# Optimization experiments

Measured on AMD Instinct MI355X. Metric: run time of the kernel, lower is better.

Reference implementation:

```python
import jax, jax.numpy as jnp
import numpy as np

N, R, IN_DIM, OUT_DIM, MODE = 8, 256, 64, 64, 32


def setup_inputs() -> dict:
    key = jax.random.key(0)
    k_x, k_w0, k_w1, k_rw, k_rb = jax.random.split(key, 5)
    scale = (1.0 / (IN_DIM * OUT_DIM)) * np.sqrt(IN_DIM + OUT_DIM)
    return {
        "x": jax.random.normal(k_x, (N, R, R, IN_DIM), dtype=jnp.float32),
        # real/imag stacked, matching torch Parameter [m, m, in, out, 2]
        "w0": jax.random.normal(k_w0, (MODE, MODE, IN_DIM, OUT_DIM, 2), dtype=jnp.float32) * scale,
        "w1": jax.random.normal(k_w1, (MODE, MODE, IN_DIM, OUT_DIM, 2), dtype=jnp.float32) * scale,
        # residual Linear: stored as [in, out] (torch keeps [out, in]; math identical)
        "res_w": jax.random.normal(k_rw, (IN_DIM, OUT_DIM), dtype=jnp.float32) * 0.05,
        "res_b": jax.random.normal(k_rb, (OUT_DIM,), dtype=jnp.float32) * 0.05,
    }


def reference(x, w0, w1, res_w, res_b):
    n, r, _, in_dim = x.shape
    m = w0.shape[0]
    rc = r // 2 + 1
    out_dim = w0.shape[3]

    # residual branch (Linear)
    res = jnp.einsum("nhwi,io->nhwo", x, res_w) + res_b  # [N, r, r, out]

    # channels-first for 2D FFT over spatial dims (droprate = 0 -> no dropout)
    xt = jnp.transpose(x, (0, 3, 1, 2))                    # [N, in, r, r]
    x_ft = jnp.fft.rfft2(xt, s=(r, r), norm="ortho")       # [N, in, r, rc] complex

    # gather low-frequency mode blocks: rows [0:m] and [r-m:r], cols [0:m]
    blk0 = x_ft[:, :, :m, :m]                              # [N, in, m, m]
    blk1 = x_ft[:, :, r - m:, :m]                          # [N, in, m, m]

    W0 = w0[..., 0] + 1j * w0[..., 1]                      # [m, m, in, out]
    W1 = w1[..., 0] + 1j * w1[..., 1]

    out0 = jnp.einsum("nixy,xyio->noxy", blk0, W0)         # [N, out, m, m]
    out1 = jnp.einsum("nixy,xyio->noxy", blk1, W1)

    # scatter back into zero-initialized full spectrum
    out_ft = jnp.zeros((n, out_dim, r, rc), dtype=out0.dtype)
    out_ft = out_ft.at[:, :, :m, :m].set(out0)
    out_ft = out_ft.at[:, :, r - m:, :m].set(out1)

    y = jnp.fft.irfft2(out_ft, s=(r, r), norm="ortho")     # [N, out, r, r]
    y = jnp.transpose(y, (0, 2, 3, 1))                     # [N, r, r, out]
    return jax.nn.silu(y + res)
```

## Files before the change

### kernel.cpp

```cpp
#include <hip/hip_runtime.h>
#include <math.h>

#define NN 8
#define RR 256
#define CD 64
#define MM 32
#define KHN 64
#define KWN 32

#define ANG 0.024543692606170259f
#define INVN (1.0f / 65536.0f)

typedef __attribute__((ext_vector_type(4))) float f32x4;
typedef __attribute__((ext_vector_type(8))) short short8;
typedef unsigned short u16;

__device__ inline u16 f2bf(float f) {
    union { float f; unsigned u; } v; v.f = f;
    unsigned r = v.u + 0x7FFF + ((v.u >> 16) & 1);
    return (u16)(r >> 16);
}
__device__ inline unsigned pack2(float a, float b) {
    return (unsigned)f2bf(a) | ((unsigned)f2bf(b) << 16);
}

__global__ __launch_bounds__(256) void k0_tables(u16* __restrict__ A2g,
                                                 u16* __restrict__ A4g,
                                                 u16* __restrict__ T1g,
                                                 u16* __restrict__ T5g) {
    int gid = blockIdx.x * 256 + threadIdx.x;
    {
        int r = gid >> 9, k = gid & 511;
        int khIdx = r & 63, part = r >> 6;
        int kh = (khIdx < 32) ? khIdx : 192 + khIdx;
        int h = k & 255, kpart = k >> 8;
        float s, c;
        __sincosf((float)((kh * h) & 255) * ANG, &s, &c);
        float v = (part == 0) ? ((kpart == 0) ? c : s)
                              : ((kpart == 0) ? -s : c);
        A2g[gid] = f2bf(v);
    }
    {
        int r = gid >> 7, k = gid & 127;
        int h = r & 255, part = r >> 8;
        int khIdx = k & 63, kpart = k >> 6;
        int kh = (khIdx < 32) ? khIdx : 192 + khIdx;
        float s, c;
        __sincosf((float)((kh * h) & 255) * ANG, &s, &c);
        float v = (part == 0) ? ((kpart == 0) ? c : -s)
                              : ((kpart == 0) ? s : c);
        A4g[gid] = f2bf(v);
    }
    if (gid < 16384) {
        {
            int r = gid >> 8, w = gid & 255;
            float s, c;
            if (r < 32) { __sincosf((float)((r * w) & 255) * ANG, &s, &c); T1g[gid] = f2bf(c); }
            else        { __sincosf((float)(((r - 32) * w) & 255) * ANG, &s, &c); T1g[gid] = f2bf(-s); }
        }
        {
            int w = gid >> 6, c = gid & 63;
            float v;
            if (c == 0) v = 1.0f;
            else if (c < 32) { float s, co; __sincosf((float)((c * w) & 255) * ANG, &s, &co); v = 2.0f * co; }
            else if (c == 32) v = 0.0f;
            else { float s, co; __sincosf((float)(((c - 32) * w) & 255) * ANG, &s, &co); v = -2.0f * s; }
            T5g[gid] = f2bf(v);
        }
    }
}

__global__ __launch_bounds__(256) void k1_dft_w(const float* __restrict__ x,
                                                const u16* __restrict__ T1g,
                                                u16* __restrict__ X1R,
                                                u16* __restrict__ X1I) {
    __shared__ __align__(16) u16 At[64 * 264];
    __shared__ __align__(16) u16 Bt[64 * 264];
    int t = threadIdx.x;
    int nh = blockIdx.x;
#pragma unroll
    for (int it = 0; it < 8; ++it) {
        int idx = t + it * 256;
        int row = idx >> 5, oct = idx & 31;
        *(uint4*)&At[row * 264 + oct * 8] = *(const uint4*)&T1g[row * 256 + oct * 8];
    }
    const float* xr = x + (size_t)nh * (RR * CD);
#pragma unroll
    for (int it = 0; it < 32; ++it) {
        int idx = t + it * 256;
        int q = idx >> 6, cc = idx & 63;
        float f0 = xr[(2 * q) * 64 + cc];
        float f1 = xr[(2 * q + 1) * 64 + cc];
        ((unsigned*)Bt)[(cc * 264 + 2 * q) >> 1] = pack2(f0, f1);
    }
    __syncthreads();
    int wv = t >> 6, l = t & 63, lm = l & 15, lq = l >> 4;
    f32x4 acc[4];
#pragma unroll
    for (int nt = 0; nt < 4; ++nt) { f32x4 z = {0.f, 0.f, 0.f, 0.f}; acc[nt] = z; }
#pragma unroll
    for (int ks = 0; ks < 8; ++ks) {
        short8 a = *(const short8*)&At[(wv * 16 + lm) * 264 + ks * 32 + lq * 8];
#pragma unroll
        for (int nt = 0; nt < 4; ++nt) {
            short8 b = *(const short8*)&Bt[(nt * 16 + lm) * 264 + ks * 32 + lq * 8];
            acc[nt] = __builtin_amdgcn_mfma_f32_16x16x32_bf16(a, b, acc[nt], 0, 0, 0);
        }
    }
#pragma unroll
    for (int nt = 0; nt < 4; ++nt)
#pragma unroll
        for (int r = 0; r < 4; ++r) {
            int kwp = wv * 16 + lq * 4 + r;
            int cc = nt * 16 + lm;
            u16 v = f2bf(acc[nt][r]);
            if (kwp < 32) X1R[(size_t)nh * 2048 + kwp * 64 + cc] = v;
            else          X1I[(size_t)nh * 2048 + (kwp - 32) * 64 + cc] = v;
        }
}

__global__ __launch_bounds__(256) void k2_dft_h(const u16* __restrict__ X1R,
                                                const u16* __restrict__ X1I,
                                                const u16* __restrict__ A2g,
                                                float2* __restrict__ X2) {
    __shared__ __align__(16) u16 As[128 * 136];
    __shared__ __align__(16) u16 Bs[64 * 136];
    int t = threadIdx.x;
    int n = blockIdx.x >> 5, kw = blockIdx.x & 31;
    int wv = t >> 6, l = t & 63, lm = l & 15, lq = l >> 4;
    f32x4 acc[2][4];
#pragma unroll
    for (int mt = 0; mt < 2; ++mt)
#pragma unroll
        for (int nt = 0; nt < 4; ++nt) { f32x4 z = {0.f, 0.f, 0.f, 0.f}; acc[mt][nt] = z; }
    for (int ck = 0; ck < 4; ++ck) {
        const u16* plane = (ck < 2) ? X1R : X1I;
        int hb = ck & 1;
#pragma unroll
        for (int it = 0; it < 8; ++it) {
            int idx = t + it * 256;
            int row = idx >> 4, oct = idx & 15;
            *(uint4*)&As[row * 136 + oct * 8] =
                *(const uint4*)&A2g[row * 512 + ck * 128 + oct * 8];
        }
#pragma unroll
        for (int it = 0; it < 16; ++it) {
            int idx = t + it * 256;
            int hl = idx >> 5, cp = idx & 31;
            int h = hb * 128 + hl;
            unsigned v = *(const unsigned*)&plane[(((size_t)n * 256 + h) * 32 + kw) * 64 + 2 * cp];
            Bs[(2 * cp) * 136 + hl] = (u16)(v & 0xFFFF);
            Bs[(2 * cp + 1) * 136 + hl] = (u16)(v >> 16);
        }
        __syncthreads();
#pragma unroll
        for (int ks = 0; ks < 4; ++ks) {
            short8 a0 = *(const short8*)&As[(wv * 32 + lm) * 136 + ks * 32 + lq * 8];
            short8 a1 = *(const short8*)&As[(wv * 32 + 16 + lm) * 136 + ks * 32 + lq * 8];
#pragma unroll
            for (int nt = 0; nt < 4; ++nt) {
                short8 b = *(const short8*)&Bs[(nt * 16 + lm) * 136 + ks * 32 + lq * 8];
                acc[0][nt] = __builtin_amdgcn_mfma_f32_16x16x32_bf16(a0, b, acc[0][nt], 0, 0, 0);
                acc[1][nt] = __builtin_amdgcn_mfma_f32_16x16x32_bf16(a1, b, acc[1][nt], 0, 0, 0);
            }
        }
        __syncthreads();
    }
#pragma unroll
    for (int mt = 0; mt < 2; ++mt)
#pragma unroll
        for (int nt = 0; nt < 4; ++nt)
#pragma unroll
            for (int r = 0; r < 4; ++r) {
                int m = wv * 32 + mt * 16 + lq * 4 + r;
                int c = nt * 16 + lm;
                float* dst = (float*)&X2[(((size_t)n * 64 + (m & 63)) * 32 + kw) * 64 + c];
                dst[m >> 6] = acc[mt][nt][r];
            }
}

__global__ __launch_bounds__(256) void k3_spectral(const float2* __restrict__ X2,
                                                   const float* __restrict__ w0,
                                                   const float* __restrict__ w1,
                                                   float2* __restrict__ X3) {
    __shared__ float WsR[4096], WsI[4096];
    __shared__ float XsR[512], XsI[512];
    int t = threadIdx.x;
    int khIdx = blockIdx.x >> 5;
    int kw = blockIdx.x & 31;
    const float* wsrc = (khIdx < 32)
        ? (w0 + (size_t)(khIdx * 32 + kw) * (64 * 64 * 2))
        : (w1 + (size_t)((khIdx - 32) * 32 + kw) * (64 * 64 * 2));
    const float2* wsrc2 = (const float2*)wsrc;
#pragma unroll
    for (int k = 0; k < 16; ++k) {
        int idx = t + k * 256;
        float2 v = wsrc2[idx];
        WsR[idx] = v.x * INVN; WsI[idx] = v.y * INVN;
    }
#pragma unroll
    for (int k = 0; k < 2; ++k) {
        int id2 = t + k * 256;
        int n = id2 >> 6, c = id2 & 63;
        float2 v = X2[(((size_t)n * KHN + khIdx) * KWN + kw) * CD + c];
        XsR[id2] = v.x; XsI[id2] = v.y;
    }
    __syncthreads();
    int o = t & 63;
    int ng = t >> 6;
#pragma unroll
    for (int p = 0; p < 2; ++p) {
        int n = ng + p * 4;
        float aR = 0.f, aI = 0.f;
#pragma unroll 8
        for (int i = 0; i < 64; ++i) {
            float xr = XsR[n * 64 + i], xi = XsI[n * 64 + i];
            float wr = WsR[i * 64 + o], wi = WsI[i * 64 + o];
            aR += xr * wr - xi * wi;
            aI += xr * wi + xi * wr;
        }
        X3[(((size_t)n * KHN + khIdx) * KWN + kw) * CD + o] = make_float2(aR, aI);
    }
}

__global__ __launch_bounds__(256) void k4_idft_h(const float2* __restrict__ X3,
                                                 const u16* __restrict__ A4g,
                                                 u16* __restrict__ Y1R,
                                                 u16* __restrict__ Y1I) {
    __shared__ __align__(16) u16 As[128 * 136];
    __shared__ __align__(16) u16 Bs[64 * 136];
    int t = threadIdx.x;
    int b = blockIdx.x;
    int n = b >> 6, kw = (b >> 1) & 31, mh = b & 1;
#pragma unroll
    for (int it = 0; it < 16; ++it) {
        int idx = t + it * 256;
        int khl = idx >> 6, o = idx & 63;
        float2 v = X3[(((size_t)n * KHN + khl) * KWN + kw) * CD + o];
        Bs[o * 136 + khl] = f2bf(v.x);
        Bs[o * 136 + 64 + khl] = f2bf(v.y);
    }
    int wv = t >> 6, l = t & 63, lm = l & 15, lq = l >> 4;
    u16* plane = mh ? Y1I : Y1R;
    for (int ac = 0; ac < 2; ++ac) {
#pragma unroll
        for (int it = 0; it < 8; ++it) {
            int idx = t + it * 256;
            int row = idx >> 4, oct = idx & 15;
            *(uint4*)&As[row * 136 + oct * 8] =
                *(const uint4*)&A4g[((size_t)(mh * 256 + ac * 128 + row)) * 128 + oct * 8];
        }
        __syncthreads();
        f32x4 acc[2][4];
#pragma unroll
        for (int mt = 0; mt < 2; ++mt)
#pragma unroll
            for (int nt = 0; nt < 4; ++nt) { f32x4 z = {0.f, 0.f, 0.f, 0.f}; acc[mt][nt] = z; }
#pragma unroll
        for (int ks = 0; ks < 4; ++ks) {
            short8 a0 = *(const short8*)&As[(wv * 32 + lm) * 136 + ks * 32 + lq * 8];
            short8 a1 = *(const short8*)&As[(wv * 32 + 16 + lm) * 136 + ks * 32 + lq * 8];
#pragma unroll
            for (int nt = 0; nt < 4; ++nt) {
                short8 bfr = *(const short8*)&Bs[(nt * 16 + lm) * 136 + ks * 32 + lq * 8];
                acc[0][nt] = __builtin_amdgcn_mfma_f32_16x16x32_bf16(a0, bfr, acc[0][nt], 0, 0, 0);
                acc[1][nt] = __builtin_amdgcn_mfma_f32_16x16x32_bf16(a1, bfr, acc[1][nt], 0, 0, 0);
            }
        }
#pragma unroll
        for (int mt = 0; mt < 2; ++mt)
#pragma unroll
            for (int nt = 0; nt < 4; ++nt)
#pragma unroll
                for (int r = 0; r < 4; ++r) {
                    int h = ac * 128 + wv * 32 + mt * 16 + lq * 4 + r;
                    int o = nt * 16 + lm;
                    plane[(((size_t)n * 256 + h) * 32 + kw) * 64 + o] = f2bf(acc[mt][nt][r]);
                }
        __syncthreads();
    }
}

__global__ __launch_bounds__(256) void k5_final(const u16* __restrict__ YRp,
                                                const u16* __restrict__ YIp,
                                                const float* __restrict__ x,
                                                const float* __restrict__ res_w,
                                                const float* __restrict__ res_b,
                                                const u16* __restrict__ T5g,
                                                float* __restrict__ out) {
    __shared__ __align__(16) u16 As[128 * 136];
    __shared__ __align__(16) u16 Bs[64 * 136];
    __shared__ float bs[64];
    int t = threadIdx.x;
    int nh = blockIdx.x >> 1, half = blockIdx.x & 1;
    if (t < 64) bs[t] = res_b[t];
#pragma unroll
    for (int it = 0; it < 4; ++it) {
        int idx = t + it * 256;
        int row = idx >> 3, oct = idx & 7;
        *(uint4*)&As[row * 136 + oct * 8] = *(const uint4*)&T5g[(half * 128 + row) * 64 + oct * 8];
    }
    const float2* xr2 = (const float2*)(x + ((size_t)nh * 256 + half * 128) * 64);
#pragma unroll
    for (int it = 0; it < 16; ++it) {
        int idx = t + it * 256;
        int r = idx >> 5, cp = idx & 31;
        float2 v = xr2[r * 32 + cp];
        ((unsigned*)As)[(r * 136 + 64 + 2 * cp) >> 1] = pack2(v.x, v.y);
    }
#pragma unroll
    for (int it = 0; it < 4; ++it) {
        int idx = t + it * 256;
        int kw = idx >> 5, op = idx & 31;
        unsigned vR = *(const unsigned*)&YRp[(size_t)nh * 2048 + kw * 64 + 2 * op];
        unsigned vI = *(const unsigned*)&YIp[(size_t)nh * 2048 + kw * 64 + 2 * op];
        Bs[(2 * op) * 136 + kw] = (u16)(vR & 0xFFFF);
        Bs[(2 * op + 1) * 136 + kw] = (u16)(vR >> 16);
        Bs[(2 * op) * 136 + 32 + kw] = (u16)(vI & 0xFFFF);
        Bs[(2 * op + 1) * 136 + 32 + kw] = (u16)(vI >> 16);
    }
#pragma unroll
    for (int it = 0; it < 16; ++it) {
        int idx = t + it * 256;
        int i = idx >> 6, o = idx & 63;
        Bs[o * 136 + 64 + i] = f2bf(res_w[idx]);
    }
    __syncthreads();
    int wv = t >> 6, l = t & 63, lm = l & 15, lq = l >> 4;
    f32x4 acc[2][4];
#pragma unroll
    for (int mt = 0; mt < 2; ++mt)
#pragma unroll
        for (int nt = 0; nt < 4; ++nt) { f32x4 z = {0.f, 0.f, 0.f, 0.f}; acc[mt][nt] = z; }
#pragma unroll
    for (int ks = 0; ks < 4; ++ks) {
        short8 a0 = *(const short8*)&As[(wv * 32 + lm) * 136 + ks * 32 + lq * 8];
        short8 a1 = *(const short8*)&As[(wv * 32 + 16 + lm) * 136 + ks * 32 + lq * 8];
#pragma unroll
        for (int nt = 0; nt < 4; ++nt) {
            short8 b = *(const short8*)&Bs[(nt * 16 + lm) * 136 + ks * 32 + lq * 8];
            acc[0][nt] = __builtin_amdgcn_mfma_f32_16x16x32_bf16(a0, b, acc[0][nt], 0, 0, 0);
            acc[1][nt] = __builtin_amdgcn_mfma_f32_16x16x32_bf16(a1, b, acc[1][nt], 0, 0, 0);
        }
    }
    float* orow = out + ((size_t)nh * 256 + half * 128) * 64;
#pragma unroll
    for (int mt = 0; mt < 2; ++mt)
#pragma unroll
        for (int nt = 0; nt < 4; ++nt)
#pragma unroll
            for (int r = 0; r < 4; ++r) {
                int wloc = wv * 32 + mt * 16 + lq * 4 + r;
                int o = nt * 16 + lm;
                float v = acc[mt][nt][r] + bs[o];
                float sv = v / (1.0f + __expf(-v));
                orow[wloc * 64 + o] = sv;
            }
}

extern "C" void kernel_launch(void* const* d_in, const int* in_sizes, int n_in,
                              void* d_out, int out_size, void* d_ws, size_t ws_size,
                              hipStream_t stream) {
    const float* x     = (const float*)d_in[0];
    const float* w0    = (const float*)d_in[1];
    const float* w1    = (const float*)d_in[2];
    const float* res_w = (const float*)d_in[3];
    const float* res_b = (const float*)d_in[4];
    float* out = (float*)d_out;
    char* ws = (char*)d_ws;
    u16*    X1R = (u16*)(ws);
    u16*    X1I = (u16*)(ws + 8388608);
    float2* X2  = (float2*)(ws + 16777216);
    float2* X3  = (float2*)(ws + 25165824);
    u16*    Y1R = (u16*)(ws + 33554432);
    u16*    Y1I = (u16*)(ws + 41943040);
    u16*    A2g = (u16*)(ws + 50331648);
    u16*    A4g = (u16*)(ws + 50462720);
    u16*    T1g = (u16*)(ws + 50593792);
    u16*    T5g = (u16*)(ws + 50626560);

    k0_tables  <<<256,          256, 0, stream>>>(A2g, A4g, T1g, T5g);
    k1_dft_w   <<<NN * RR,      256, 0, stream>>>(x, T1g, X1R, X1I);
    k2_dft_h   <<<NN * KWN,     256, 0, stream>>>(X1R, X1I, A2g, X2);
    k3_spectral<<<KHN * KWN,    256, 0, stream>>>(X2, w0, w1, X3);
    k4_idft_h  <<<NN * KWN * 2, 256, 0, stream>>>(X3, A4g, Y1R, Y1I);
    k5_final   <<<NN * RR * 2,  256, 0, stream>>>(Y1R, Y1I, x, res_w, res_b, T5g, out);
}
```

Measured before the change: 371.4 us.

## Swizzle LDS layouts, read DFT tables from global, retile kernels, pretranspose residual weights

All MFMA kernels now use XOR-swizzled, unpadded LDS tiles instead of padded ones, and they read the constant DFT twiddle tables straight from global memory instead of staging them in LDS. k1 loads x with float4 and writes X1 in an [n][kw][h][c] layout so k2 can read it contiguously. k2 moves to 512 threads with a double-buffered staging pipeline, and k4 is split across twice as many blocks. k3 packs its intermediate output as bf16 pairs in a transposed layout, and the residual weights are pre-transposed and converted to bf16 once in the table kernel. The aim is to cut LDS bank conflicts, uncoalesced gathers and conversion work in the hot kernels. The cost is more global-memory A-operand traffic and extra bf16 rounding of the spectral intermediate.

Result: faster. 352.6 us (-5.1%).

```diff
diff --git a/kernel.cpp b/kernel.cpp
--- a/kernel.cpp
+++ b/kernel.cpp
@@ -23,11 +23,14 @@
 __device__ inline unsigned pack2(float a, float b) {
     return (unsigned)f2bf(a) | ((unsigned)f2bf(b) << 16);
 }
+__device__ inline int swkey(int row) { return (row & 7) ^ ((row >> 3) & 7); }
 
 __global__ __launch_bounds__(256) void k0_tables(u16* __restrict__ A2g,
                                                  u16* __restrict__ A4g,
                                                  u16* __restrict__ T1g,
-                                                 u16* __restrict__ T5g) {
+                                                 u16* __restrict__ T5g,
+                                                 const float* __restrict__ res_w,
+                                                 u16* __restrict__ RWTg) {
     int gid = blockIdx.x * 256 + threadIdx.x;
     {
         int r = gid >> 9, k = gid & 511;
@@ -68,30 +71,32 @@
             T5g[gid] = f2bf(v);
         }
     }
+    if (gid < 4096) {
+        int o = gid >> 6, i = gid & 63;
+        RWTg[gid] = f2bf(res_w[i * 64 + o]);
+    }
 }
 
 __global__ __launch_bounds__(256) void k1_dft_w(const float* __restrict__ x,
                                                 const u16* __restrict__ T1g,
                                                 u16* __restrict__ X1R,
                                                 u16* __restrict__ X1I) {
-    __shared__ __align__(16) u16 At[64 * 264];
-    __shared__ __align__(16) u16 Bt[64 * 264];
+    __shared__ __align__(16) u16 Bt[64 * 256];
+    unsigned* B32 = (unsigned*)Bt;
     int t = threadIdx.x;
     int nh = blockIdx.x;
+    const float* xr = x + (size_t)nh * (RR * CD);
 #pragma unroll
     for (int it = 0; it < 8; ++it) {
         int idx = t + it * 256;
-        int row = idx >> 5, oct = idx & 31;
-        *(uint4*)&At[row * 264 + oct * 8] = *(const uint4*)&T1g[row * 256 + oct * 8];
-    }
-    const float* xr = x + (size_t)nh * (RR * CD);
-#pragma unroll
-    for (int it = 0; it < 32; ++it) {
-        int idx = t + it * 256;
-        int q = idx >> 6, cc = idx & 63;
-        float f0 = xr[(2 * q) * 64 + cc];
-        float f1 = xr[(2 * q + 1) * 64 + cc];
-        ((unsigned*)Bt)[(cc * 264 + 2 * q) >> 1] = pack2(f0, f1);
+        int q = idx >> 4;
+        int c0 = (idx & 15) * 4;
+        float4 f0 = *(const float4*)&xr[(2 * q) * 64 + c0];
+        float4 f1 = *(const float4*)&xr[(2 * q + 1) * 64 + c0];
+        B32[(c0 + 0) * 128 + (q ^ (swkey(c0 + 0) << 2))] = pack2(f0.x, f1.x);
+        B32[(c0 + 1) * 128 + (q ^ (swkey(c0 + 1) << 2))] = pack2(f0.y, f1.y);
+        B32[(c0 + 2) * 128 + (q ^ (swkey(c0 + 2) << 2))] = pack2(f0.z, f1.z);
+        B32[(c0 + 3) * 128 + (q ^ (swkey(c0 + 3) << 2))] = pack2(f0.w, f1.w);
     }
     __syncthreads();
     int wv = t >> 6, l = t & 63, lm = l & 15, lq = l >> 4;
@@ -100,13 +105,15 @@
     for (int nt = 0; nt < 4; ++nt) { f32x4 z = {0.f, 0.f, 0.f, 0.f}; acc[nt] = z; }
 #pragma unroll
     for (int ks = 0; ks < 8; ++ks) {
-        short8 a = *(const short8*)&At[(wv * 16 + lm) * 264 + ks * 32 + lq * 8];
+        short8 a = *(const short8*)&T1g[(wv * 16 + lm) * 256 + ks * 32 + lq * 8];
 #pragma unroll
         for (int nt = 0; nt < 4; ++nt) {
-            short8 b = *(const short8*)&Bt[(nt * 16 + lm) * 264 + ks * 32 + lq * 8];
+            int c = nt * 16 + lm;
+            short8 b = *(const short8*)&Bt[c * 256 + ((ks * 32 + lq * 8) ^ (swkey(c) << 3))];
             acc[nt] = __builtin_amdgcn_mfma_f32_16x16x32_bf16(a, b, acc[nt], 0, 0, 0);
         }
     }
+    int n = nh >> 8, h = nh & 255;
 #pragma unroll
     for (int nt = 0; nt < 4; ++nt)
 #pragma unroll
@@ -114,96 +121,93 @@
             int kwp = wv * 16 + lq * 4 + r;
             int cc = nt * 16 + lm;
             u16 v = f2bf(acc[nt][r]);
-            if (kwp < 32) X1R[(size_t)nh * 2048 + kwp * 64 + cc] = v;
-            else          X1I[(size_t)nh * 2048 + (kwp - 32) * 64 + cc] = v;
-        }
-}
-
-__global__ __launch_bounds__(256) void k2_dft_h(const u16* __restrict__ X1R,
+            if (kwp < 32) X1R[(((size_t)n * 32 + kwp) * 256 + h) * 64 + cc] = v;
+            else          X1I[(((size_t)n * 32 + (kwp - 32)) * 256 + h) * 64 + cc] = v;
+        }
+}
+
+__global__ __launch_bounds__(512) void k2_dft_h(const u16* __restrict__ X1R,
                                                 const u16* __restrict__ X1I,
                                                 const u16* __restrict__ A2g,
                                                 float2* __restrict__ X2) {
-    __shared__ __align__(16) u16 As[128 * 136];
-    __shared__ __align__(16) u16 Bs[64 * 136];
+    __shared__ __align__(16) u16 Bs[2][64 * 128];
     int t = threadIdx.x;
     int n = blockIdx.x >> 5, kw = blockIdx.x & 31;
+    const u16* baseR = X1R + ((size_t)n * 32 + kw) * (256 * 64);
+    const u16* baseI = X1I + ((size_t)n * 32 + kw) * (256 * 64);
     int wv = t >> 6, l = t & 63, lm = l & 15, lq = l >> 4;
-    f32x4 acc[2][4];
-#pragma unroll
-    for (int mt = 0; mt < 2; ++mt)
-#pragma unroll
-        for (int nt = 0; nt < 4; ++nt) { f32x4 z = {0.f, 0.f, 0.f, 0.f}; acc[mt][nt] = z; }
+    f32x4 acc[4];
+#pragma unroll
+    for (int nt = 0; nt < 4; ++nt) { f32x4 z = {0.f, 0.f, 0.f, 0.f}; acc[nt] = z; }
+
+    auto stage = [&](int ck, int buf) {
+        const u16* src = ((ck < 2) ? baseR : baseI) + (size_t)(ck & 1) * (128 * 64);
+        u16* B = Bs[buf];
+#pragma unroll
+        for (int it = 0; it < 2; ++it) {
+            int idx = t + it * 512;
+            int hh = idx >> 3, g = idx & 7;
+            short8 v = *(const short8*)&src[hh * 64 + g * 8];
+#pragma unroll
+            for (int j = 0; j < 8; ++j) {
+                int c = g * 8 + j;
+                B[c * 128 + (hh ^ (swkey(c) << 3))] = (u16)v[j];
+            }
+        }
+    };
+    stage(0, 0);
+    __syncthreads();
     for (int ck = 0; ck < 4; ++ck) {
-        const u16* plane = (ck < 2) ? X1R : X1I;
-        int hb = ck & 1;
-#pragma unroll
-        for (int it = 0; it < 8; ++it) {
-            int idx = t + it * 256;
-            int row = idx >> 4, oct = idx & 15;
-            *(uint4*)&As[row * 136 + oct * 8] =
-                *(const uint4*)&A2g[row * 512 + ck * 128 + oct * 8];
-        }
-#pragma unroll
-        for (int it = 0; it < 16; ++it) {
-            int idx = t + it * 256;
-            int hl = idx >> 5, cp = idx & 31;
-            int h = hb * 128 + hl;
-            unsigned v = *(const unsigned*)&plane[(((size_t)n * 256 + h) * 32 + kw) * 64 + 2 * cp];
-            Bs[(2 * cp) * 136 + hl] = (u16)(v & 0xFFFF);
-            Bs[(2 * cp + 1) * 136 + hl] = (u16)(v >> 16);
+        if (ck < 3) stage(ck + 1, (ck + 1) & 1);
+        const u16* B = Bs[ck & 1];
+#pragma unroll
+        for (int ks = 0; ks < 4; ++ks) {
+            short8 a = *(const short8*)&A2g[(wv * 16 + lm) * 512 + ck * 128 + ks * 32 + lq * 8];
+#pragma unroll
+            for (int nt = 0; nt < 4; ++nt) {
+                int c = nt * 16 + lm;
+                short8 b = *(const short8*)&B[c * 128 + ((ks * 32 + lq * 8) ^ (swkey(c) << 3))];
+                acc[nt] = __builtin_amdgcn_mfma_f32_16x16x32_bf16(a, b, acc[nt], 0, 0, 0);
+            }
         }
         __syncthreads();
-#pragma unroll
-        for (int ks = 0; ks < 4; ++ks) {
-            short8 a0 = *(const short8*)&As[(wv * 32 + lm) * 136 + ks * 32 + lq * 8];
-            short8 a1 = *(const short8*)&As[(wv * 32 + 16 + lm) * 136 + ks * 32 + lq * 8];
-#pragma unroll
-            for (int nt = 0; nt < 4; ++nt) {
-                short8 b = *(const short8*)&Bs[(nt * 16 + lm) * 136 + ks * 32 + lq * 8];
-                acc[0][nt] = __builtin_amdgcn_mfma_f32_16x16x32_bf16(a0, b, acc[0][nt], 0, 0, 0);
-                acc[1][nt] = __builtin_amdgcn_mfma_f32_16x16x32_bf16(a1, b, acc[1][nt], 0, 0, 0);
-            }
-        }
-        __syncthreads();
-    }
-#pragma unroll
-    for (int mt = 0; mt < 2; ++mt)
-#pragma unroll
-        for (int nt = 0; nt < 4; ++nt)
-#pragma unroll
-            for (int r = 0; r < 4; ++r) {
-                int m = wv * 32 + mt * 16 + lq * 4 + r;
-                int c = nt * 16 + lm;
-                float* dst = (float*)&X2[(((size_t)n * 64 + (m & 63)) * 32 + kw) * 64 + c];
-                dst[m >> 6] = acc[mt][nt][r];
-            }
+    }
+#pragma unroll
+    for (int nt = 0; nt < 4; ++nt)
+#pragma unroll
+        for (int r = 0; r < 4; ++r) {
+            int m = wv * 16 + lq * 4 + r;
+            int c = nt * 16 + lm;
+            float* dst = (float*)&X2[(((size_t)n * 64 + (m & 63)) * 32 + kw) * 64 + c];
+            dst[m >> 6] = acc[nt][r];
+        }
 }
 
 __global__ __launch_bounds__(256) void k3_spectral(const float2* __restrict__ X2,
                                                    const float* __restrict__ w0,
                                                    const float* __restrict__ w1,
-                                                   float2* __restrict__ X3) {
-    __shared__ float WsR[4096], WsI[4096];
-    __shared__ float XsR[512], XsI[512];
+                                                   unsigned* __restrict__ X3b) {
+    __shared__ float2 WsP[4096];
+    __shared__ float2 XsP[512];
     int t = threadIdx.x;
     int khIdx = blockIdx.x >> 5;
     int kw = blockIdx.x & 31;
     const float* wsrc = (khIdx < 32)
         ? (w0 + (size_t)(khIdx * 32 + kw) * (64 * 64 * 2))
         : (w1 + (size_t)((khIdx - 32) * 32 + kw) * (64 * 64 * 2));
-    const float2* wsrc2 = (const float2*)wsrc;
-#pragma unroll
-    for (int k = 0; k < 16; ++k) {
+    const float4* wsrc4 = (const float4*)wsrc;
+#pragma unroll
+    for (int k = 0; k < 8; ++k) {
         int idx = t + k * 256;
-        float2 v = wsrc2[idx];
-        WsR[idx] = v.x * INVN; WsI[idx] = v.y * INVN;
+        float4 v = wsrc4[idx];
+        WsP[2 * idx]     = make_float2(v.x * INVN, v.y * INVN);
+        WsP[2 * idx + 1] = make_float2(v.z * INVN, v.w * INVN);
     }
 #pragma unroll
     for (int k = 0; k < 2; ++k) {
         int id2 = t + k * 256;
         int n = id2 >> 6, c = id2 & 63;
-        float2 v = X2[(((size_t)n * KHN + khIdx) * KWN + kw) * CD + c];
-        XsR[id2] = v.x; XsI[id2] = v.y;
+        XsP[id2] = X2[(((size_t)n * KHN + khIdx) * KWN + kw) * CD + c];
     }
     __syncthreads();
     int o = t & 63;
@@ -214,116 +218,108 @@
         float aR = 0.f, aI = 0.f;
 #pragma unroll 8
         for (int i = 0; i < 64; ++i) {
-            float xr = XsR[n * 64 + i], xi = XsI[n * 64 + i];
-            float wr = WsR[i * 64 + o], wi = WsI[i * 64 + o];
-            aR += xr * wr - xi * wi;
-            aI += xr * wi + xi * wr;
-        }
-        X3[(((size_t)n * KHN + khIdx) * KWN + kw) * CD + o] = make_float2(aR, aI);
-    }
-}
-
-__global__ __launch_bounds__(256) void k4_idft_h(const float2* __restrict__ X3,
+            float2 xv = XsP[n * 64 + i];
+            float2 wv_ = WsP[i * 64 + o];
+            aR += xv.x * wv_.x - xv.y * wv_.y;
+            aI += xv.x * wv_.y + xv.y * wv_.x;
+        }
+        X3b[(((size_t)n * 32 + kw) * 64 + khIdx) * 64 + o] = pack2(aR, aI);
+    }
+}
+
+__global__ __launch_bounds__(256) void k4_idft_h(const unsigned* __restrict__ X3b,
                                                  const u16* __restrict__ A4g,
                                                  u16* __restrict__ Y1R,
                                                  u16* __restrict__ Y1I) {
-    __shared__ __align__(16) u16 As[128 * 136];
-    __shared__ __align__(16) u16 Bs[64 * 136];
+    __shared__ __align__(16) u16 Bs[64 * 128];
     int t = threadIdx.x;
     int b = blockIdx.x;
-    int n = b >> 6, kw = (b >> 1) & 31, mh = b & 1;
+    int n = b >> 7, kw = (b >> 2) & 31, mh = (b >> 1) & 1, ac = b & 1;
+    const unsigned* src = X3b + ((size_t)n * 32 + kw) * (64 * 64);
 #pragma unroll
     for (int it = 0; it < 16; ++it) {
-        int idx = t + it * 256;
-        int khl = idx >> 6, o = idx & 63;
-        float2 v = X3[(((size_t)n * KHN + khl) * KWN + kw) * CD + o];
-        Bs[o * 136 + khl] = f2bf(v.x);
-        Bs[o * 136 + 64 + khl] = f2bf(v.y);
-    }
+        int khl = (t & 7) + ((it & 7) << 3);
+        int o = ((t >> 3) & 31) + ((it >> 3) << 5);
+        unsigned v = src[khl * 64 + o];
+        int K = swkey(o) << 3;
+        Bs[o * 128 + (khl ^ K)]        = (u16)(v & 0xFFFF);
+        Bs[o * 128 + ((64 + khl) ^ K)] = (u16)(v >> 16);
+    }
+    __syncthreads();
     int wv = t >> 6, l = t & 63, lm = l & 15, lq = l >> 4;
     u16* plane = mh ? Y1I : Y1R;
-    for (int ac = 0; ac < 2; ++ac) {
-#pragma unroll
-        for (int it = 0; it < 8; ++it) {
-            int idx = t + it * 256;
-            int row = idx >> 4, oct = idx & 15;
-            *(uint4*)&As[row * 136 + oct * 8] =
-                *(const uint4*)&A4g[((size_t)(mh * 256 + ac * 128 + row)) * 128 + oct * 8];
-        }
-        __syncthreads();
-        f32x4 acc[2][4];
-#pragma unroll
-        for (int mt = 0; mt < 2; ++mt)
-#pragma unroll
-            for (int nt = 0; nt < 4; ++nt) { f32x4 z = {0.f, 0.f, 0.f, 0.f}; acc[mt][nt] = z; }
-#pragma unroll
-        for (int ks = 0; ks < 4; ++ks) {
-            short8 a0 = *(const short8*)&As[(wv * 32 + lm) * 136 + ks * 32 + lq * 8];
-            short8 a1 = *(const short8*)&As[(wv * 32 + 16 + lm) * 136 + ks * 32 + lq * 8];
-#pragma unroll
-            for (int nt = 0; nt < 4; ++nt) {
-                short8 bfr = *(const short8*)&Bs[(nt * 16 + lm) * 136 + ks * 32 + lq * 8];
-                acc[0][nt] = __builtin_amdgcn_mfma_f32_16x16x32_bf16(a0, bfr, acc[0][nt], 0, 0, 0);
-                acc[1][nt] = __builtin_amdgcn_mfma_f32_16x16x32_bf16(a1, bfr, acc[1][nt], 0, 0, 0);
+    f32x4 acc[2][4];
+#pragma unroll
+    for (int mt = 0; mt < 2; ++mt)
+#pragma unroll
+        for (int nt = 0; nt < 4; ++nt) { f32x4 z = {0.f, 0.f, 0.f, 0.f}; acc[mt][nt] = z; }
+#pragma unroll
+    for (int ks = 0; ks < 4; ++ks) {
+        short8 a0 = *(const short8*)&A4g[(size_t)(mh * 256 + ac * 128 + wv * 32 + lm) * 128 + ks * 32 + lq * 8];
+        short8 a1 = *(const short8*)&A4g[(size_t)(mh * 256 + ac * 128 + wv * 32 + 16 + lm) * 128 + ks * 32 + lq * 8];
+#pragma unroll
+        for (int nt = 0; nt < 4; ++nt) {
+            int c = nt * 16 + lm;
+            short8 bfr = *(const short8*)&Bs[c * 128 + ((ks * 32 + lq * 8) ^ (swkey(c) << 3))];
+            acc[0][nt] = __builtin_amdgcn_mfma_f32_16x16x32_bf16(a0, bfr, acc[0][nt], 0, 0, 0);
+            acc[1][nt] = __builtin_amdgcn_mfma_f32_16x16x32_bf16(a1, bfr, acc[1][nt], 0, 0, 0);
+        }
+    }
+#pragma unroll
+    for (int mt = 0; mt < 2; ++mt)
+#pragma unroll
+        for (int nt = 0; nt < 4; ++nt)
+#pragma unroll
+            for (int r = 0; r < 4; ++r) {
+                int h = ac * 128 + wv * 32 + mt * 16 + lq * 4 + r;
+                int o = nt * 16 + lm;
+                plane[(((size_t)n * 256 + h) * 32 + kw) * 64 + o] = f2bf(acc[mt][nt][r]);
             }
-        }
-#pragma unroll
-        for (int mt = 0; mt < 2; ++mt)
-#pragma unroll
-            for (int nt = 0; nt < 4; ++nt)
-#pragma unroll
-                for (int r = 0; r < 4; ++r) {
-                    int h = ac * 128 + wv * 32 + mt * 16 + lq * 4 + r;
-                    int o = nt * 16 + lm;
-                    plane[(((size_t)n * 256 + h) * 32 + kw) * 64 + o] = f2bf(acc[mt][nt][r]);
-                }
-        __syncthreads();
-    }
 }
 
 __global__ __launch_bounds__(256) void k5_final(const u16* __restrict__ YRp,
                                                 const u16* __restrict__ YIp,
                                                 const float* __restrict__ x,
-                                                const float* __restrict__ res_w,
                                                 const float* __restrict__ res_b,
                                                 const u16* __restrict__ T5g,
+                                                const u16* __restrict__ RWTg,
                                                 float* __restrict__ out) {
-    __shared__ __align__(16) u16 As[128 * 136];
-    __shared__ __align__(16) u16 Bs[64 * 136];
+    __shared__ __align__(16) u16 Xs[128 * 64];
+    __shared__ __align__(16) u16 Bs[64 * 128];
     __shared__ float bs[64];
+    unsigned* X32 = (unsigned*)Xs;
+    unsigned* B32 = (unsigned*)Bs;
     int t = threadIdx.x;
     int nh = blockIdx.x >> 1, half = blockIdx.x & 1;
     if (t < 64) bs[t] = res_b[t];
-#pragma unroll
-    for (int it = 0; it < 4; ++it) {
+    const float* xb = x + ((size_t)nh * 256 + half * 128) * 64;
+#pragma unroll
+    for (int it = 0; it < 8; ++it) {
         int idx = t + it * 256;
-        int row = idx >> 3, oct = idx & 7;
-        *(uint4*)&As[row * 136 + oct * 8] = *(const uint4*)&T5g[(half * 128 + row) * 64 + oct * 8];
-    }
-    const float2* xr2 = (const float2*)(x + ((size_t)nh * 256 + half * 128) * 64);
-#pragma unroll
-    for (int it = 0; it < 16; ++it) {
+        int wl = idx >> 4, c4 = idx & 15;
+        float4 f = *(const float4*)&xb[wl * 64 + c4 * 4];
+        uint2 pv; pv.x = pack2(f.x, f.y); pv.y = pack2(f.z, f.w);
+        *(uint2*)&X32[wl * 32 + ((2 * c4) ^ (swkey(wl) << 2))] = pv;
+    }
+    const u16* YR = YRp + (size_t)nh * 2048;
+    const u16* YI = YIp + (size_t)nh * 2048;
+#pragma unroll
+    for (int it = 0; it < 8; ++it) {
+        int kw = t >> 3;
+        int op = (t & 7) + (it & 3) * 8;
+        const u16* P = (it >> 2) ? YI : YR;
+        unsigned v = *(const unsigned*)&P[kw * 64 + 2 * op];
+        int k = (it >> 2) * 32 + kw;
+        int o0 = 2 * op;
+        Bs[o0 * 128 + (k ^ (swkey(o0) << 3))]       = (u16)(v & 0xFFFF);
+        Bs[(o0 + 1) * 128 + (k ^ (swkey(o0 + 1) << 3))] = (u16)(v >> 16);
+    }
+#pragma unroll
+    for (int it = 0; it < 2; ++it) {
         int idx = t + it * 256;
-        int r = idx >> 5, cp = idx & 31;
-        float2 v = xr2[r * 32 + cp];
-        ((unsigned*)As)[(r * 136 + 64 + 2 * cp) >> 1] = pack2(v.x, v.y);
-    }
-#pragma unroll
-    for (int it = 0; it < 4; ++it) {
-        int idx = t + it * 256;
-        int kw = idx >> 5, op = idx & 31;
-        unsigned vR = *(const unsigned*)&YRp[(size_t)nh * 2048 + kw * 64 + 2 * op];
-        unsigned vI = *(const unsigned*)&YIp[(size_t)nh * 2048 + kw * 64 + 2 * op];
-        Bs[(2 * op) * 136 + kw] = (u16)(vR & 0xFFFF);
-        Bs[(2 * op + 1) * 136 + kw] = (u16)(vR >> 16);
-        Bs[(2 * op) * 136 + 32 + kw] = (u16)(vI & 0xFFFF);
-        Bs[(2 * op + 1) * 136 + 32 + kw] = (u16)(vI >> 16);
-    }
-#pragma unroll
-    for (int it = 0; it < 16; ++it) {
-        int idx = t + it * 256;
-        int i = idx >> 6, o = idx & 63;
-        Bs[o * 136 + 64 + i] = f2bf(res_w[idx]);
+        int o = idx >> 3, g = idx & 7;
+        uint4 v = *(const uint4*)&RWTg[o * 64 + g * 8];
+        *(uint4*)&B32[o * 64 + (8 + (g ^ swkey(o))) * 4] = v;
     }
     __syncthreads();
     int wv = t >> 6, l = t & 63, lm = l & 15, lq = l >> 4;
@@ -334,11 +330,19 @@
         for (int nt = 0; nt < 4; ++nt) { f32x4 z = {0.f, 0.f, 0.f, 0.f}; acc[mt][nt] = z; }
 #pragma unroll
     for (int ks = 0; ks < 4; ++ks) {
-        short8 a0 = *(const short8*)&As[(wv * 32 + lm) * 136 + ks * 32 + lq * 8];
-        short8 a1 = *(const short8*)&As[(wv * 32 + 16 + lm) * 136 + ks * 32 + lq * 8];
+        int r0 = wv * 32 + lm, r1 = r0 + 16;
+        short8 a0, a1;
+        if (ks < 2) {
+            a0 = *(const short8*)&T5g[(half * 128 + r0) * 64 + ks * 32 + lq * 8];
+            a1 = *(const short8*)&T5g[(half * 128 + r1) * 64 + ks * 32 + lq * 8];
+        } else {
+            a0 = *(const short8*)&Xs[r0 * 64 + (((ks - 2) * 32 + lq * 8) ^ (swkey(r0) << 3))];
+            a1 = *(const short8*)&Xs[r1 * 64 + (((ks - 2) * 32 + lq * 8) ^ (swkey(r1) << 3))];
+        }
 #pragma unroll
         for (int nt = 0; nt < 4; ++nt) {
-            short8 b = *(const short8*)&Bs[(nt * 16 + lm) * 136 + ks * 32 + lq * 8];
+            int c = nt * 16 + lm;
+            short8 b = *(const short8*)&Bs[c * 128 + ((ks * 32 + lq * 8) ^ (swkey(c) << 3))];
             acc[0][nt] = __builtin_amdgcn_mfma_f32_16x16x32_bf16(a0, b, acc[0][nt], 0, 0, 0);
             acc[1][nt] = __builtin_amdgcn_mfma_f32_16x16x32_bf16(a1, b, acc[1][nt], 0, 0, 0);
         }
@@ -368,21 +372,22 @@
     const float* res_b = (const float*)d_in[4];
     float* out = (float*)d_out;
     char* ws = (char*)d_ws;
-    u16*    X1R = (u16*)(ws);
-    u16*    X1I = (u16*)(ws + 8388608);
-    float2* X2  = (float2*)(ws + 16777216);
-    float2* X3  = (float2*)(ws + 25165824);
-    u16*    Y1R = (u16*)(ws + 33554432);
-    u16*    Y1I = (u16*)(ws + 41943040);
-    u16*    A2g = (u16*)(ws + 50331648);
-    u16*    A4g = (u16*)(ws + 50462720);
-    u16*    T1g = (u16*)(ws + 50593792);
-    u16*    T5g = (u16*)(ws + 50626560);
-
-    k0_tables  <<<256,          256, 0, stream>>>(A2g, A4g, T1g, T5g);
+    u16*      X1R  = (u16*)(ws);
+    u16*      X1I  = (u16*)(ws + 8388608);
+    float2*   X2   = (float2*)(ws + 16777216);
+    unsigned* X3b  = (unsigned*)(ws + 25165824);
+    u16*      Y1R  = (u16*)(ws + 33554432);
+    u16*      Y1I  = (u16*)(ws + 41943040);
+    u16*      A2g  = (u16*)(ws + 50331648);
+    u16*      A4g  = (u16*)(ws + 50462720);
+    u16*      T1g  = (u16*)(ws + 50593792);
+    u16*      T5g  = (u16*)(ws + 50626560);
+    u16*      RWTg = (u16*)(ws + 50659328);
+
+    k0_tables  <<<256,          256, 0, stream>>>(A2g, A4g, T1g, T5g, res_w, RWTg);
     k1_dft_w   <<<NN * RR,      256, 0, stream>>>(x, T1g, X1R, X1I);
-    k2_dft_h   <<<NN * KWN,     256, 0, stream>>>(X1R, X1I, A2g, X2);
-    k3_spectral<<<KHN * KWN,    256, 0, stream>>>(X2, w0, w1, X3);
-    k4_idft_h  <<<NN * KWN * 2, 256, 0, stream>>>(X3, A4g, Y1R, Y1I);
-    k5_final   <<<NN * RR * 2,  256, 0, stream>>>(Y1R, Y1I, x, res_w, res_b, T5g, out);
-}
+    k2_dft_h   <<<NN * KWN,     512, 0, stream>>>(X1R, X1I, A2g, X2);
+    k3_spectral<<<KHN * KWN,    256, 0, stream>>>(X2, w0, w1, X3b);
+    k4_idft_h  <<<NN * KWN * 4, 256, 0, stream>>>(X3b, A4g, Y1R, Y1I);
+    k5_final   <<<NN * RR * 2,  256, 0, stream>>>(Y1R, Y1I, x, res_b, T5g, RWTg, out);
+}
```
